# Kernel tuning notes

Measured on AMD Instinct MI355X. Metric: run time of the kernel, lower is better.

Reference implementation:

```python
import jax, jax.numpy as jnp
import numpy as np

B, S, D = 16, 512, 512
UPS = 3
THRESH = 1.0
SM1, NT1 = 1.0, 0.0
TAIL = 0.45
SM2, NT2 = 0.25, 0.01


def setup_inputs() -> dict:
    key = jax.random.key(0)
    ks = jax.random.split(key, 20)
    r = lambda k, sh, s: (jax.random.normal(k, sh, jnp.float32) * s)
    H4 = 4 * D
    return {
        "hidden": jax.random.normal(ks[0], (B, S, D), jnp.float32),
        "mask": jnp.ones((B, 1, S), jnp.float32),
        # Conv1d(D, D, 3): torch weight [out, in, k]
        "conv_w": r(ks[1], (D, D, 3), 0.03),
        "conv_b": jnp.zeros((D,), jnp.float32),
        # Linear(D, 1)
        "out_w": r(ks[2], (1, D), 0.05),
        "out_b": jnp.zeros((1,), jnp.float32),
        # ConvTranspose1d(D, D, 3, stride=3): torch weight [in, out, k]
        "up_w": r(ks[3], (D, D, 3), 0.03),
        "up_b": jnp.zeros((D,), jnp.float32),
        # BiLSTM(D -> D), torch gate order i,f,g,o
        "w_ih_f": r(ks[4], (H4, D), 0.03), "w_hh_f": r(ks[5], (H4, D), 0.03),
        "b_ih_f": jnp.zeros((H4,), jnp.float32), "b_hh_f": jnp.zeros((H4,), jnp.float32),
        "w_ih_b": r(ks[6], (H4, D), 0.03), "w_hh_b": r(ks[7], (H4, D), 0.03),
        "b_ih_b": jnp.zeros((H4,), jnp.float32), "b_hh_b": jnp.zeros((H4,), jnp.float32),
        # Linear(2D, 1)
        "out2_w": r(ks[8], (1, 2 * D), 0.05),
        "out2_b": jnp.zeros((1,), jnp.float32),
    }


def _lstm_dir(x, w_ih, w_hh, b_ih, b_hh, reverse):
    # x: [B, T, D] -> h: [B, T, H]
    Bx = x.shape[0]
    H = w_hh.shape[1]
    xg = jnp.einsum('btd,gd->btg', x, w_ih) + b_ih + b_hh  # [B,T,4H]
    xg = jnp.swapaxes(xg, 0, 1)  # [T,B,4H]

    def step(carry, g):
        h, c = carry
        g = g + h @ w_hh.T
        i, f, gg, o = jnp.split(g, 4, axis=-1)
        c = jax.nn.sigmoid(f) * c + jax.nn.sigmoid(i) * jnp.tanh(gg)
        h = jax.nn.sigmoid(o) * jnp.tanh(c)
        return (h, c), h

    init = (jnp.zeros((Bx, H), x.dtype), jnp.zeros((Bx, H), x.dtype))
    _, hs = jax.lax.scan(step, init, xg, reverse=reverse)
    return jnp.swapaxes(hs, 0, 1)


def _cif(h, alphas):
    # h: [B, T, D], alphas: [B, T] -> padded fired frames [B, T, D]
    Bz, Tz, Dz = h.shape

    def step(carry, inp):
        integrate, frame = carry
        alpha, h_t = inp
        dist = 1.0 - integrate
        integrate = integrate + alpha
        fire_val = integrate
        fire = integrate >= THRESH
        integrate = jnp.where(fire, integrate - 1.0, integrate)
        cur = jnp.where(fire, dist, alpha)
        frame_out = frame + cur[:, None] * h_t
        frame_next = jnp.where(fire[:, None], (alpha - cur)[:, None] * h_t, frame_out)
        return (integrate, frame_next), (fire_val, frame_out)

    init = (jnp.zeros((Bz,), h.dtype), jnp.zeros((Bz, Dz), h.dtype))
    xs = (jnp.swapaxes(alphas, 0, 1), jnp.swapaxes(h, 0, 1))
    _, (fires, frames) = jax.lax.scan(step, init, xs)
    fires = jnp.swapaxes(fires, 0, 1)    # [B,T]
    frames = jnp.swapaxes(frames, 0, 1)  # [B,T,D]
    # ragged gather of fired frames, packed to the front (vectorized)
    fire_mask = fires >= THRESH
    dest = jnp.where(fire_mask, jnp.cumsum(fire_mask.astype(jnp.int32), axis=1) - 1, Tz)
    embeds = jnp.zeros((Bz, Tz + 1, Dz), frames.dtype)
    embeds = embeds.at[jnp.arange(Bz)[:, None], dest].set(frames)
    return embeds[:, :Tz]  # drop dump slot


def _cif_wo_hidden(alphas):
    th = THRESH - 0.0001

    def step(integrate, alpha):
        integrate = integrate + alpha
        out = integrate
        integrate = jnp.where(integrate >= th, integrate - th, integrate)
        return integrate, out

    init = jnp.zeros((alphas.shape[0],), alphas.dtype)
    _, fires = jax.lax.scan(step, init, jnp.swapaxes(alphas, 0, 1))
    return jnp.swapaxes(fires, 0, 1)


def reference(hidden, mask, conv_w, conv_b, out_w, out_b, up_w, up_b,
              w_ih_f, w_hh_f, b_ih_f, b_hh_f, w_ih_b, w_hh_b, b_ih_b, b_hh_b,
              out2_w, out2_b):
    Bz, Sz, Dz = hidden.shape
    ctx = jnp.swapaxes(hidden, 1, 2)  # [B,D,S]
    # cif alphas branch: pad(1,1) + Conv1d(k=3) + relu
    q = jax.lax.conv_general_dilated(ctx, conv_w, (1,), [(1, 1)],
                                     dimension_numbers=('NCH', 'OIH', 'NCH'))
    q = jax.nn.relu(q + conv_b[None, :, None])
    out = jnp.swapaxes(q, 1, 2)  # [B,S,D]
    alphas = jax.nn.sigmoid(out @ out_w.T + out_b)        # [B,S,1]
    alphas = jax.nn.relu(alphas * SM1 - NT1)
    mk = jnp.swapaxes(mask, -1, -2)                        # [B,S,1]
    alphas = (alphas * mk)[..., 0]                         # [B,S]
    mk2 = mk[..., 0]                                       # [B,S]

    # tail_process_fn
    zeros_t = jnp.zeros((Bz, 1), alphas.dtype)
    ones_t = jnp.ones((Bz, 1), alphas.dtype)
    tail_mask = jnp.concatenate([ones_t, mk2], 1) - jnp.concatenate([mk2, zeros_t], 1)
    alphas = jnp.concatenate([alphas, zeros_t], 1) + tail_mask * TAIL  # [B,S+1]
    h = jnp.concatenate([hidden, jnp.zeros((Bz, 1, Dz), hidden.dtype)], 1)
    token_num = jnp.floor(jnp.sum(alphas, -1))

    acoustic_embeds = _cif(h, alphas)  # [B,S+1,D] (padded; original slices to max token_num)

    # get_timestamp: ConvTranspose1d stride==kernel==3 (non-overlapping)
    up = jnp.einsum('bit,iok->botk', ctx, up_w).reshape(Bz, Dz, Sz * UPS)
    up = up + up_b[None, :, None]
    xu = jnp.swapaxes(up, 1, 2)  # [B,3S,D]
    hf = _lstm_dir(xu, w_ih_f, w_hh_f, b_ih_f, b_hh_f, reverse=False)
    hb = _lstm_dir(xu, w_ih_b, w_hh_b, b_ih_b, b_hh_b, reverse=True)
    hcat = jnp.concatenate([hf, hb], -1)  # [B,3S,2D]
    us = jax.nn.sigmoid(hcat @ out2_w.T + out2_b)
    us = jax.nn.relu(us * SM2 - NT2)  # [B,3S,1]
    m_up = jnp.swapaxes(jnp.tile(mask, (1, UPS, 1)), -1, -2).reshape(Bz, -1)  # [B,3S]
    us_alphas = us[..., 0] * m_up
    us_alphas = us_alphas * (token_num / jnp.sum(us_alphas, -1))[:, None]
    us_peaks = _cif_wo_hidden(us_alphas)
    return acoustic_embeds, token_num, alphas, us_alphas, us_peaks
```

## Files before the change

kernel.cpp:

```cpp
#include <hip/hip_runtime.h>
#include <math.h>

constexpr int Bz = 16;
constexpr int Sz = 512;
constexpr int Dz = 512;
constexpr int T1 = Sz + 1;
constexpr int TU = Sz * 3;
constexpr float THRESHc = 1.0f;
constexpr float SM1c = 1.0f, NT1c = 0.0f;
constexpr float TAILc = 0.45f;
constexpr float SM2c = 0.25f, NT2c = 0.01f;

constexpr int GD = 16;

constexpr int EMB_OFF = 0;
constexpr int TOK_OFF = Bz * T1 * Dz;
constexpr int ALUT_OFF = TOK_OFF + Bz;
constexpr int USA_OFF = ALUT_OFF + Bz * T1;
constexpr int USP_OFF = USA_OFF + Bz * TU;

typedef short bf16x8 __attribute__((ext_vector_type(8)));
typedef float f32x4 __attribute__((ext_vector_type(4)));
typedef unsigned long long u64;

__device__ __forceinline__ float sigm(float x) { return 1.0f / (1.0f + expf(-x)); }
__device__ __forceinline__ float fsigm(float x) { return 1.0f / (1.0f + __expf(-x)); }
__device__ __forceinline__ float ftanh(float x) {
    float e = __expf(2.0f * x);
    return 1.0f - 2.0f / (e + 1.0f);
}
__device__ __forceinline__ unsigned short f2bf(float f) {
    unsigned u = __float_as_uint(f);
    return (unsigned short)((u + 0x7fffu + ((u >> 16) & 1u)) >> 16);
}

__global__ void k_transpose_convw(const float* __restrict__ cw, float* __restrict__ wt) {
    __shared__ float tile[64][65];
    int dt = blockIdx.x * 64, ct = blockIdx.y * 64;
    int tx = threadIdx.x & 63, ty = threadIdx.x >> 6;
    for (int r = ty; r < 64; r += 4)
        tile[r][tx] = cw[(dt + r) * 1536 + ct + tx];
    __syncthreads();
    for (int r = ty; r < 64; r += 4)
        wt[(ct + r) * 512 + dt + tx] = tile[tx][r];
}

__global__ void k_transpose_upw(const float* __restrict__ uw, float* __restrict__ upt) {
    __shared__ float tile[64][65];
    int it = blockIdx.x * 64, ct = blockIdx.y * 64;
    int tx = threadIdx.x & 63, ty = threadIdx.x >> 6;
    for (int r = ty; r < 64; r += 4)
        tile[r][tx] = uw[(it + r) * 1536 + ct + tx];
    __syncthreads();
    for (int r = ty; r < 64; r += 4) {
        int c = ct + r;
        int k = c % 3, o = c / 3;
        upt[(k * 512 + o) * 512 + it + tx] = tile[tx][r];
    }
}

__global__ void k_gconst(const float* __restrict__ wih_f, const float* __restrict__ bih_f,
                         const float* __restrict__ bhh_f, const float* __restrict__ wih_b,
                         const float* __restrict__ bih_b, const float* __restrict__ bhh_b,
                         const float* __restrict__ upb, float* __restrict__ gconst) {
    int g = blockIdx.x * 256 + threadIdx.x;
    int dir = g >> 11, gg = g & 2047;
    const float* wih = dir ? wih_b : wih_f;
    const float* bi = dir ? bih_b : bih_f;
    const float* bh = dir ? bhh_b : bhh_f;
    float s = bi[gg] + bh[gg];
    const float4* w4 = (const float4*)(wih + (size_t)gg * 512);
    const float4* u4 = (const float4*)upb;
    for (int o = 0; o < 128; ++o) {
        float4 w = w4[o], u = u4[o];
        s += w.x * u.x + w.y * u.y + w.z * u.z + w.w * u.w;
    }
    gconst[g] = s;
}

__global__ void k_M(const float* __restrict__ wih_f, const float* __restrict__ wih_b,
                    const float* __restrict__ upt, unsigned short* __restrict__ Mh) {
    __shared__ float As[32][68];
    __shared__ float Bs[32][68];
    int z = blockIdx.z;
    int dir = z / 3, k = z % 3;
    const float* A = dir ? wih_b : wih_f;
    const float* Bt = upt + (size_t)k * 262144;
    int g0 = blockIdx.y * 64, i0 = blockIdx.x * 64;
    int tid = threadIdx.x;
    int tx = tid & 15, ty = tid >> 4;
    float acc[4][4] = {};
    for (int k0 = 0; k0 < 512; k0 += 32) {
#pragma unroll
        for (int e = 0; e < 8; ++e) {
            int idx = e * 256 + tid;
            int ko = idx & 31, gl = idx >> 5;
            As[ko][gl] = A[(size_t)(g0 + gl) * 512 + k0 + ko];
        }
#pragma unroll
        for (int e = 0; e < 8; ++e) {
            int idx = e * 256 + tid;
            int il = idx & 63, ko = idx >> 6;
            Bs[ko][il] = Bt[(size_t)(k0 + ko) * 512 + i0 + il];
        }
        __syncthreads();
#pragma unroll
        for (int ko = 0; ko < 32; ++ko) {
            float4 a = *(const float4*)&As[ko][ty * 4];
            float4 b = *(const float4*)&Bs[ko][tx * 4];
            acc[0][0] += a.x * b.x; acc[0][1] += a.x * b.y; acc[0][2] += a.x * b.z; acc[0][3] += a.x * b.w;
            acc[1][0] += a.y * b.x; acc[1][1] += a.y * b.y; acc[1][2] += a.y * b.z; acc[1][3] += a.y * b.w;
            acc[2][0] += a.z * b.x; acc[2][1] += a.z * b.y; acc[2][2] += a.z * b.z; acc[2][3] += a.z * b.w;
            acc[3][0] += a.w * b.x; acc[3][1] += a.w * b.y; acc[3][2] += a.w * b.z; acc[3][3] += a.w * b.w;
        }
        __syncthreads();
    }
#pragma unroll
    for (int r = 0; r < 4; ++r) {
        ushort4 wh;
        wh.x = f2bf(acc[r][0]); wh.y = f2bf(acc[r][1]);
        wh.z = f2bf(acc[r][2]); wh.w = f2bf(acc[r][3]);
        *(ushort4*)&Mh[((size_t)(z * 2048 + g0 + ty * 4 + r)) * 512 + i0 + tx * 4] = wh;
    }
}

__global__ void k_Hbf(const float* __restrict__ hidden, unsigned short* __restrict__ Hs) {
    int i = blockIdx.x * 256 + threadIdx.x;
    float4 v = *(const float4*)&hidden[(size_t)i * 4];
    ushort4 h4;
    h4.x = f2bf(v.x); h4.y = f2bf(v.y); h4.z = f2bf(v.z); h4.w = f2bf(v.w);
    *(ushort4*)&Hs[(size_t)i * 4] = h4;
}

__global__ void k_conv_alpha(const float* __restrict__ hidden, const float* __restrict__ wt,
                             const float* __restrict__ cb, const float* __restrict__ ow,
                             const float* __restrict__ ob, const float* __restrict__ mask,
                             float* __restrict__ alph_s) {
    __shared__ float hs[18 * 512];
    __shared__ float red[16][257];
    int b = blockIdx.x, s0 = blockIdx.y * 16;
    int tid = threadIdx.x;
#pragma unroll
    for (int e = 0; e < 36; ++e) {
        int idx = e * 256 + tid;
        int r = idx >> 9, i = idx & 511;
        int s = s0 + r - 1;
        hs[idx] = (s >= 0 && s < Sz) ? hidden[((size_t)b * Sz + s) * Dz + i] : 0.f;
    }
    __syncthreads();
    float acc0[16] = {}, acc1[16] = {};
    int d0 = tid, d1 = tid + 256;
    for (int i = 0; i < 512; ++i) {
        float w00 = wt[(i * 3 + 0) * 512 + d0];
        float w01 = wt[(i * 3 + 1) * 512 + d0];
        float w02 = wt[(i * 3 + 2) * 512 + d0];
        float w10 = wt[(i * 3 + 0) * 512 + d1];
        float w11 = wt[(i * 3 + 1) * 512 + d1];
        float w12 = wt[(i * 3 + 2) * 512 + d1];
        float hv[18];
#pragma unroll
        for (int r = 0; r < 18; ++r) hv[r] = hs[r * 512 + i];
#pragma unroll
        for (int j = 0; j < 16; ++j) {
            acc0[j] += hv[j] * w00 + hv[j + 1] * w01 + hv[j + 2] * w02;
            acc1[j] += hv[j] * w10 + hv[j + 1] * w11 + hv[j + 2] * w12;
        }
    }
    float cb0 = cb[d0], cb1 = cb[d1], ow0 = ow[d0], ow1 = ow[d1];
#pragma unroll
    for (int j = 0; j < 16; ++j)
        red[j][tid] = fmaxf(acc0[j] + cb0, 0.f) * ow0 + fmaxf(acc1[j] + cb1, 0.f) * ow1;
    __syncthreads();
    for (int off = 128; off >= 1; off >>= 1) {
        if (tid < off) {
#pragma unroll
            for (int j = 0; j < 16; ++j) red[j][tid] += red[j][tid + off];
        }
        __syncthreads();
    }
    if (tid < 16) {
        float v = red[tid][0] + ob[0];
        float a = sigm(v);
        a = fmaxf(a * SM1c - NT1c, 0.f);
        a *= mask[b * Sz + s0 + tid];
        alph_s[b * Sz + s0 + tid] = a;
    }
}

__global__ void k_cif_scan(const float* __restrict__ alph_s, const float* __restrict__ mask,
                           float* __restrict__ out, float* __restrict__ sc_cur,
                           float* __restrict__ sc_res, int* __restrict__ sc_dst) {
    __shared__ float sa[16][T1];
    int tid = threadIdx.x;
    for (int idx = tid; idx < 16 * T1; idx += 256) {
        int b = idx / T1, t = idx % T1;
        float a = (t < Sz) ? alph_s[b * Sz + t] : 0.f;
        float mp = (t == 0) ? 1.f : mask[b * Sz + t - 1];
        float mc = (t < Sz) ? mask[b * Sz + t] : 0.f;
        sa[b][t] = a + (mp - mc) * TAILc;
    }
    __syncthreads();
    if (tid < 16) {
        int b = tid;
        float integ = 0.f, sum = 0.f;
        int nf = 0;
        for (int t = 0; t < T1; ++t) {
            float a = sa[b][t];
            out[ALUT_OFF + b * T1 + t] = a;
            sum += a;
            float dist = 1.f - integ;
            integ += a;
            bool fire = (integ >= THRESHc);
            float cur = fire ? dist : a;
            sc_cur[b * T1 + t] = cur;
            sc_res[b * T1 + t] = fire ? (a - cur) : 0.f;
            sc_dst[b * T1 + t] = fire ? (nf++) : -1;
            if (fire) integ -= 1.f;
        }
        out[TOK_OFF + b] = floorf(sum);
    }
}

__global__ void k_cif_frames(const float* __restrict__ hidden, const float* __restrict__ sc_cur,
                             const float* __restrict__ sc_res, const int* __restrict__ sc_dst,
                             float* __restrict__ out) {
    __shared__ float cu[T1], re[T1];
    __shared__ int dsx[T1];
    int b = blockIdx.x, d = blockIdx.y * 256 + threadIdx.x;
    for (int t = threadIdx.x; t < T1; t += 256) {
        cu[t] = sc_cur[b * T1 + t];
        re[t] = sc_res[b * T1 + t];
        dsx[t] = sc_dst[b * T1 + t];
    }
    __syncthreads();
    float frame = 0.f;
    for (int t = 0; t < T1; ++t) {
        float ht = (t < Sz) ? hidden[((size_t)b * Sz + t) * Dz + d] : 0.f;
        float f = frame + cu[t] * ht;
        int dst = dsx[t];
        if (dst >= 0) {
            out[EMB_OFF + ((size_t)b * T1 + dst) * Dz + d] = f;
            frame = re[t] * ht;
        } else {
            frame = f;
        }
    }
}

__global__ void __launch_bounds__(256, 1)
k_lstm(const unsigned short* __restrict__ Mh, const unsigned short* __restrict__ Hs,
       const float* __restrict__ whh_f, const float* __restrict__ whh_b,
       const float* __restrict__ gconst, const float* __restrict__ w2,
       unsigned short* hX, float* part, int* prog) {
    __shared__ unsigned short hbh[16 * 512];
    __shared__ float xch[3 * 256];

    const int wg = blockIdx.x;
    const int dir = wg >> 5, slice = wg & 31;
    const int d0 = slice * GD;
    const int tid = threadIdx.x;
    const int wv = tid >> 6;
    const int l = tid & 63;
    const int colb = l & 15;
    const int khi = l >> 4;
    const float* whh = dir ? whh_b : whh_f;

    bf16x8 whA[16];
    {
        const float* wr = whh + (size_t)(wv * 512 + d0 + colb) * 512 + khi * 8;
#pragma unroll
        for (int m = 0; m < 16; ++m) {
            float4 a = *(const float4*)(wr + m * 32);
            float4 b = *(const float4*)(wr + m * 32 + 4);
            union { unsigned short u[8]; bf16x8 v; } hh;
            hh.u[0] = f2bf(a.x); hh.u[1] = f2bf(a.y); hh.u[2] = f2bf(a.z); hh.u[3] = f2bf(a.w);
            hh.u[4] = f2bf(b.x); hh.u[5] = f2bf(b.y); hh.u[6] = f2bf(b.z); hh.u[7] = f2bf(b.w);
            whA[m] = hh.v;
        }
    }

    f32x4 bias;
    float w2v[4], cst[4] = {0.f, 0.f, 0.f, 0.f};
#pragma unroll
    for (int j = 0; j < 4; ++j) {
        bias[j] = gconst[dir * 2048 + wv * 512 + d0 + khi * 4 + j];
        w2v[j] = w2[dir * 512 + d0 + khi * 4 + j];
    }
    int* myprog = prog + (dir * 32 + slice) * 16;
    const int* pollp = prog + (dir * 32 + (l & 31)) * 16;

    auto idot = [&](int n) -> f32x4 {
        int t = dir ? (TU - 1 - n) : n;
        int s = t / 3, k = t - 3 * s;
        const unsigned short* ma = Mh + ((size_t)((dir * 3 + k) * 2048 + wv * 512 + d0 + colb)) * 512 + khi * 8;
        const unsigned short* xa = Hs + ((size_t)(colb * 512 + s)) * 512 + khi * 8;
        f32x4 a = bias;
#pragma unroll
        for (int m = 0; m < 16; ++m) {
            bf16x8 A = *(const bf16x8*)(ma + m * 32);
            bf16x8 B = *(const bf16x8*)(xa + m * 32);
            a = __builtin_amdgcn_mfma_f32_16x16x32_bf16(A, B, a, 0, 0, 0);
        }
        return a;
    };

    f32x4 accA = idot(0);

    for (int n = 0; n < TU; ++n) {
        int t = dir ? (TU - 1 - n) : n;
        if (n > 0) {
            {
                int it = 0;
                while (true) {
                    int v;
                    asm volatile("global_load_dword %0, %1, off sc0 sc1\n\ts_waitcnt vmcnt(0)"
                                 : "=v"(v) : "v"(pollp));
                    if (__ballot(v >= n) == ~0ull) break;
                    if (++it > (1 << 15)) break;
                    __builtin_amdgcn_s_sleep(1);
                }
            }
            int slot = (n - 1) & 1;
            const unsigned short* hb = hX + (size_t)((dir * 2 + slot) * 16) * 512;
            bf16x8 hg[4];
#pragma unroll
            for (int j = 0; j < 4; ++j)
                asm volatile("global_load_dwordx4 %0, %1, off sc0 sc1"
                             : "=v"(hg[j]) : "v"(hb + j * 2048 + tid * 8));
            asm volatile("s_waitcnt vmcnt(0)" ::: "memory");
            __builtin_amdgcn_sched_barrier(0);
#pragma unroll
            for (int j = 0; j < 4; ++j) {
                int row = j * 4 + wv;
                *(bf16x8*)&hbh[row * 512 + ((l ^ (row & 7)) * 8)] = hg[j];
            }
            __syncthreads();
#pragma unroll
            for (int m = 0; m < 16; ++m) {
                int G = m * 4 + khi;
                bf16x8 B = *(const bf16x8*)&hbh[colb * 512 + ((G ^ (colb & 7)) * 8)];
                accA = __builtin_amdgcn_mfma_f32_16x16x32_bf16(whA[m], B, accA, 0, 0, 0);
            }
        }
        if (wv != 0) {
#pragma unroll
            for (int j = 0; j < 4; ++j)
                xch[(wv - 1) * 256 + (khi * 4 + j) * 16 + colb] = accA[j];
        }
        __syncthreads();
        if (wv == 0) {
            unsigned short h4[4];
            float p = 0.f;
#pragma unroll
            for (int j = 0; j < 4; ++j) {
                int rr = khi * 4 + j;
                float gi = accA[j];
                float gf = xch[0 * 256 + rr * 16 + colb];
                float gg = xch[1 * 256 + rr * 16 + colb];
                float go = xch[2 * 256 + rr * 16 + colb];
                float c2 = fsigm(gf) * cst[j] + fsigm(gi) * ftanh(gg);
                cst[j] = c2;
                float h = fsigm(go) * ftanh(c2);
                h4[j] = f2bf(h);
                p += h * w2v[j];
            }
            u64 hq = (u64)h4[0] | ((u64)h4[1] << 16) | ((u64)h4[2] << 32) | ((u64)h4[3] << 48);
            size_t hoff = ((size_t)((dir * 2 + (n & 1)) * 16 + colb)) * 512 + d0 + khi * 4;
            asm volatile("global_store_dwordx2 %0, %1, off sc0 sc1"
                         :: "v"(hX + hoff), "v"(hq) : "memory");
            p += __shfl_xor(p, 16);
            p += __shfl_xor(p, 32);
            if (l < 16)
                part[((size_t)((dir * 32 + slice) * 16) + l) * TU + t] = p;
            asm volatile("s_waitcnt vmcnt(0)" ::: "memory");
            if (l == 0) {
                int nv = n + 1;
                asm volatile("global_store_dword %0, %1, off sc0 sc1"
                             :: "v"(myprog), "v"(nv) : "memory");
            }
        }
        accA = (n + 1 < TU) ? idot(n + 1) : bias;
    }
}

__global__ void k_us_reduce(const float* __restrict__ part, const float* __restrict__ ob2,
                            const float* __restrict__ mask, float* __restrict__ usA,
                            float* __restrict__ csum) {
    int b = blockIdx.x, ch = blockIdx.y;
    int t = ch * 256 + threadIdx.x;
    float s = 0.f;
#pragma unroll 8
    for (int p = 0; p < 64; ++p) s += part[((size_t)p * Bz + b) * TU + t];
    float u = sigm(s + ob2[0]);
    float ua = fmaxf(u * SM2c - NT2c, 0.f) * mask[b * Sz + t / 3];
    usA[b * TU + t] = ua;
    __shared__ float red[256];
    red[threadIdx.x] = ua;
    __syncthreads();
    for (int off = 128; off >= 1; off >>= 1) {
        if (threadIdx.x < off) red[threadIdx.x] += red[threadIdx.x + off];
        __syncthreads();
    }
    if (threadIdx.x == 0) csum[b * 6 + ch] = red[0];
}

__global__ void k_us_scan(const float* __restrict__ usA, const float* __restrict__ csum,
                          float* __restrict__ out) {
    __shared__ float ubuf[TU];
    int b = blockIdx.x;
    for (int t = threadIdx.x; t < TU; t += 64) ubuf[t] = usA[b * TU + t];
    __syncthreads();
    if (threadIdx.x == 0) {
        float tot = 0.f;
        for (int c = 0; c < 6; ++c) tot += csum[b * 6 + c];
        float scale = out[TOK_OFF + b] / tot;
        float integ = 0.f;
        const float th = THRESHc - 0.0001f;
        for (int t = 0; t < TU; ++t) {
            float ua = ubuf[t] * scale;
            out[USA_OFF + b * TU + t] = ua;
            integ += ua;
            out[USP_OFF + b * TU + t] = integ;
            if (integ >= th) integ -= th;
        }
    }
}

extern "C" void kernel_launch(void* const* d_in, const int* in_sizes, int n_in,
                              void* d_out, int out_size, void* d_ws, size_t ws_size,
                              hipStream_t stream) {
    const float* hidden = (const float*)d_in[0];
    const float* mask   = (const float*)d_in[1];
    const float* conv_w = (const float*)d_in[2];
    const float* conv_b = (const float*)d_in[3];
    const float* out_w  = (const float*)d_in[4];
    const float* out_b  = (const float*)d_in[5];
    const float* up_w   = (const float*)d_in[6];
    const float* up_b   = (const float*)d_in[7];
    const float* w_ih_f = (const float*)d_in[8];
    const float* w_hh_f = (const float*)d_in[9];
    const float* b_ih_f = (const float*)d_in[10];
    const float* b_hh_f = (const float*)d_in[11];
    const float* w_ih_b = (const float*)d_in[12];
    const float* w_hh_b = (const float*)d_in[13];
    const float* b_ih_b = (const float*)d_in[14];
    const float* b_hh_b = (const float*)d_in[15];
    const float* out2_w = (const float*)d_in[16];
    const float* out2_b = (const float*)d_in[17];
    float* out = (float*)d_out;
    float* ws = (float*)d_ws;

    float* wt     = ws + 0;
    float* upt    = ws + 786432;
    float* part   = ws + 1572864;
    float* gconst = ws + 3145728;
    float* alph_s = ws + 3149824;
    float* sc_cur = ws + 3158016;
    float* sc_res = ws + 3166224;
    int*   sc_dst = (int*)(ws + 3174432);
    unsigned short* hX = (unsigned short*)(ws + 3182640);
    float* usA    = ws + 3199024;
    float* csum   = ws + 3223600;
    int*   prog   = (int*)(ws + 3223696);
    unsigned short* Mh = (unsigned short*)(ws + 3224720);
    unsigned short* Hs = (unsigned short*)(ws + 6370448);

    hipMemsetAsync(out, 0, (size_t)Bz * T1 * Dz * sizeof(float), stream);
    hipMemsetAsync(prog, 0, 1024 * sizeof(int), stream);

    k_transpose_convw<<<dim3(8, 24), 256, 0, stream>>>(conv_w, wt);
    k_transpose_upw<<<dim3(8, 24), 256, 0, stream>>>(up_w, upt);
    k_gconst<<<16, 256, 0, stream>>>(w_ih_f, b_ih_f, b_hh_f, w_ih_b, b_ih_b, b_hh_b, up_b, gconst);
    k_M<<<dim3(8, 32, 6), 256, 0, stream>>>(w_ih_f, w_ih_b, upt, Mh);
    k_Hbf<<<4096, 256, 0, stream>>>(hidden, Hs);
    k_conv_alpha<<<dim3(16, 32), 256, 0, stream>>>(hidden, wt, conv_b, out_w, out_b, mask, alph_s);
    k_cif_scan<<<1, 256, 0, stream>>>(alph_s, mask, out, sc_cur, sc_res, sc_dst);
    k_cif_frames<<<dim3(16, 2), 256, 0, stream>>>(hidden, sc_cur, sc_res, sc_dst, out);

    {
        void* args[] = { (void*)&Mh, (void*)&Hs, (void*)&w_hh_f, (void*)&w_hh_b,
                         (void*)&gconst, (void*)&out2_w, (void*)&hX, (void*)&part,
                         (void*)&prog };
        hipLaunchCooperativeKernel(reinterpret_cast<void*>(&k_lstm), dim3(64), dim3(256),
                                   args, 0, stream);
    }

    k_us_reduce<<<dim3(16, 6), 256, 0, stream>>>(part, out2_b, mask, usA, csum);
    k_us_scan<<<16, 64, 0, stream>>>(usA, csum, out);
}
```

Before: 10.26 ms.

## Interleave both LSTM directions per workgroup and embed step tags in exchanged data

```diff
diff --git a/kernel.cpp b/kernel.cpp
--- a/kernel.cpp
+++ b/kernel.cpp
@@ -21,6 +21,7 @@
 
 typedef short bf16x8 __attribute__((ext_vector_type(8)));
 typedef float f32x4 __attribute__((ext_vector_type(4)));
+typedef unsigned u32x4 __attribute__((ext_vector_type(4)));
 typedef unsigned long long u64;
 
 __device__ __forceinline__ float sigm(float x) { return 1.0f / (1.0f + expf(-x)); }
@@ -251,50 +252,56 @@
 k_lstm(const unsigned short* __restrict__ Mh, const unsigned short* __restrict__ Hs,
        const float* __restrict__ whh_f, const float* __restrict__ whh_b,
        const float* __restrict__ gconst, const float* __restrict__ w2,
-       unsigned short* hX, float* part, int* prog) {
-    __shared__ unsigned short hbh[16 * 512];
+       u32x4* exch, float* part) {
+    __shared__ unsigned short hbuf[16 * 512];
     __shared__ float xch[3 * 256];
 
-    const int wg = blockIdx.x;
-    const int dir = wg >> 5, slice = wg & 31;
+    const int slice = blockIdx.x;
     const int d0 = slice * GD;
     const int tid = threadIdx.x;
     const int wv = tid >> 6;
     const int l = tid & 63;
     const int colb = l & 15;
     const int khi = l >> 4;
-    const float* whh = dir ? whh_b : whh_f;
-
-    bf16x8 whA[16];
+
+    bf16x8 whF[16], whB[16];
     {
-        const float* wr = whh + (size_t)(wv * 512 + d0 + colb) * 512 + khi * 8;
+        const float* wrF = whh_f + (size_t)(wv * 512 + d0 + colb) * 512 + khi * 8;
+        const float* wrB = whh_b + (size_t)(wv * 512 + d0 + colb) * 512 + khi * 8;
 #pragma unroll
         for (int m = 0; m < 16; ++m) {
-            float4 a = *(const float4*)(wr + m * 32);
-            float4 b = *(const float4*)(wr + m * 32 + 4);
-            union { unsigned short u[8]; bf16x8 v; } hh;
-            hh.u[0] = f2bf(a.x); hh.u[1] = f2bf(a.y); hh.u[2] = f2bf(a.z); hh.u[3] = f2bf(a.w);
-            hh.u[4] = f2bf(b.x); hh.u[5] = f2bf(b.y); hh.u[6] = f2bf(b.z); hh.u[7] = f2bf(b.w);
-            whA[m] = hh.v;
-        }
-    }
-
-    f32x4 bias;
-    float w2v[4], cst[4] = {0.f, 0.f, 0.f, 0.f};
+            float4 a = *(const float4*)(wrF + m * 32);
+            float4 b = *(const float4*)(wrF + m * 32 + 4);
+            union { unsigned short u[8]; bf16x8 v; } t1;
+            t1.u[0] = f2bf(a.x); t1.u[1] = f2bf(a.y); t1.u[2] = f2bf(a.z); t1.u[3] = f2bf(a.w);
+            t1.u[4] = f2bf(b.x); t1.u[5] = f2bf(b.y); t1.u[6] = f2bf(b.z); t1.u[7] = f2bf(b.w);
+            whF[m] = t1.v;
+            a = *(const float4*)(wrB + m * 32);
+            b = *(const float4*)(wrB + m * 32 + 4);
+            union { unsigned short u[8]; bf16x8 v; } t2;
+            t2.u[0] = f2bf(a.x); t2.u[1] = f2bf(a.y); t2.u[2] = f2bf(a.z); t2.u[3] = f2bf(a.w);
+            t2.u[4] = f2bf(b.x); t2.u[5] = f2bf(b.y); t2.u[6] = f2bf(b.z); t2.u[7] = f2bf(b.w);
+            whB[m] = t2.v;
+        }
+    }
+
+    f32x4 biasF, biasB;
+    float w2F[4], w2B[4];
+    f32x4 cstF = {0.f, 0.f, 0.f, 0.f}, cstB = {0.f, 0.f, 0.f, 0.f};
 #pragma unroll
     for (int j = 0; j < 4; ++j) {
-        bias[j] = gconst[dir * 2048 + wv * 512 + d0 + khi * 4 + j];
-        w2v[j] = w2[dir * 512 + d0 + khi * 4 + j];
-    }
-    int* myprog = prog + (dir * 32 + slice) * 16;
-    const int* pollp = prog + (dir * 32 + (l & 31)) * 16;
-
-    auto idot = [&](int n) -> f32x4 {
+        biasF[j] = gconst[0 * 2048 + wv * 512 + d0 + khi * 4 + j];
+        biasB[j] = gconst[1 * 2048 + wv * 512 + d0 + khi * 4 + j];
+        w2F[j] = w2[0 * 512 + d0 + khi * 4 + j];
+        w2B[j] = w2[1 * 512 + d0 + khi * 4 + j];
+    }
+
+    auto idot = [&](int dir, int n) -> f32x4 {
         int t = dir ? (TU - 1 - n) : n;
         int s = t / 3, k = t - 3 * s;
         const unsigned short* ma = Mh + ((size_t)((dir * 3 + k) * 2048 + wv * 512 + d0 + colb)) * 512 + khi * 8;
         const unsigned short* xa = Hs + ((size_t)(colb * 512 + s)) * 512 + khi * 8;
-        f32x4 a = bias;
+        f32x4 a = dir ? biasB : biasF;
 #pragma unroll
         for (int m = 0; m < 16; ++m) {
             bf16x8 A = *(const bf16x8*)(ma + m * 32);
@@ -304,48 +311,57 @@
         return a;
     };
 
-    f32x4 accA = idot(0);
-
-    for (int n = 0; n < TU; ++n) {
-        int t = dir ? (TU - 1 - n) : n;
-        if (n > 0) {
-            {
-                int it = 0;
-                while (true) {
-                    int v;
-                    asm volatile("global_load_dword %0, %1, off sc0 sc1\n\ts_waitcnt vmcnt(0)"
-                                 : "=v"(v) : "v"(pollp));
-                    if (__ballot(v >= n) == ~0ull) break;
-                    if (++it > (1 << 15)) break;
-                    __builtin_amdgcn_s_sleep(1);
-                }
-            }
-            int slot = (n - 1) & 1;
-            const unsigned short* hb = hX + (size_t)((dir * 2 + slot) * 16) * 512;
-            bf16x8 hg[4];
+    u32x4 gS[8];
+
+    auto issue8 = [&](int d, int n) {
+        const u32x4* base = exch + (size_t)((d * 2 + ((n - 1) & 1)) * 2048) + tid * 8;
+#pragma unroll
+        for (int j = 0; j < 8; ++j)
+            asm volatile("global_load_dwordx4 %0, %1, off sc0 sc1"
+                         : "=v"(gS[j]) : "v"(base + j));
+    };
+    auto waitok = [&](int d, int n) {
+        const u32x4* base = exch + (size_t)((d * 2 + ((n - 1) & 1)) * 2048) + tid * 8;
+        unsigned tag = (unsigned)n;
+        int it = 0;
+        while (true) {
+            asm volatile("s_waitcnt vmcnt(0)" ::: "memory");
+            bool ok = true;
+#pragma unroll
+            for (int j = 0; j < 8; ++j) ok = ok && (gS[j][2] == tag);
+            if (__ballot(!ok) == 0ull) break;
+            if (++it > (1 << 13)) break;
+            __builtin_amdgcn_s_sleep(1);
+#pragma unroll
+            for (int j = 0; j < 8; ++j)
+                asm volatile("global_load_dwordx4 %0, %1, off sc0 sc1"
+                             : "=v"(gS[j]) : "v"(base + j));
+        }
+    };
+    auto unpack = [&]() {
+#pragma unroll
+        for (int j = 0; j < 8; ++j) {
+            int u = tid * 8 + j;
+            int batch = u & 15;
+            int gq = u >> 4;
+            int sw = (((gq >> 1) ^ (batch & 7)) << 3) + ((gq & 1) << 2);
+            u64 q = (u64)gS[j][0] | ((u64)gS[j][1] << 32);
+            *(u64*)&hbuf[batch * 512 + sw] = q;
+        }
+    };
+    auto hhdot = [&](const bf16x8* wh, f32x4 acc) -> f32x4 {
+#pragma unroll
+        for (int m = 0; m < 16; ++m) {
+            bf16x8 B = *(const bf16x8*)&hbuf[colb * 512 + (((m * 4 + khi) ^ (colb & 7)) << 3)];
+            acc = __builtin_amdgcn_mfma_f32_16x16x32_bf16(wh[m], B, acc, 0, 0, 0);
+        }
+        return acc;
+    };
+    auto cellphase = [&](f32x4 acc, f32x4& cst, const float* w2v, int d, int n, int t) {
+        if (wv != 0) {
 #pragma unroll
             for (int j = 0; j < 4; ++j)
-                asm volatile("global_load_dwordx4 %0, %1, off sc0 sc1"
-                             : "=v"(hg[j]) : "v"(hb + j * 2048 + tid * 8));
-            asm volatile("s_waitcnt vmcnt(0)" ::: "memory");
-            __builtin_amdgcn_sched_barrier(0);
-#pragma unroll
-            for (int j = 0; j < 4; ++j) {
-                int row = j * 4 + wv;
-                *(bf16x8*)&hbh[row * 512 + ((l ^ (row & 7)) * 8)] = hg[j];
-            }
-            __syncthreads();
-#pragma unroll
-            for (int m = 0; m < 16; ++m) {
-                int G = m * 4 + khi;
-                bf16x8 B = *(const bf16x8*)&hbh[colb * 512 + ((G ^ (colb & 7)) * 8)];
-                accA = __builtin_amdgcn_mfma_f32_16x16x32_bf16(whA[m], B, accA, 0, 0, 0);
-            }
-        }
-        if (wv != 0) {
-#pragma unroll
-            for (int j = 0; j < 4; ++j)
-                xch[(wv - 1) * 256 + (khi * 4 + j) * 16 + colb] = accA[j];
+                xch[(wv - 1) * 256 + (khi * 4 + j) * 16 + colb] = acc[j];
         }
         __syncthreads();
         if (wv == 0) {
@@ -354,7 +370,7 @@
 #pragma unroll
             for (int j = 0; j < 4; ++j) {
                 int rr = khi * 4 + j;
-                float gi = accA[j];
+                float gi = acc[j];
                 float gf = xch[0 * 256 + rr * 16 + colb];
                 float gg = xch[1 * 256 + rr * 16 + colb];
                 float go = xch[2 * 256 + rr * 16 + colb];
@@ -364,22 +380,43 @@
                 h4[j] = f2bf(h);
                 p += h * w2v[j];
             }
-            u64 hq = (u64)h4[0] | ((u64)h4[1] << 16) | ((u64)h4[2] << 32) | ((u64)h4[3] << 48);
-            size_t hoff = ((size_t)((dir * 2 + (n & 1)) * 16 + colb)) * 512 + d0 + khi * 4;
-            asm volatile("global_store_dwordx2 %0, %1, off sc0 sc1"
-                         :: "v"(hX + hoff), "v"(hq) : "memory");
+            unsigned lo = (unsigned)h4[0] | ((unsigned)h4[1] << 16);
+            unsigned hi = (unsigned)h4[2] | ((unsigned)h4[3] << 16);
+            u32x4 outv = { lo, hi, (unsigned)(n + 1), (unsigned)(n + 1) };
+            u32x4* dst = exch + (size_t)((d * 2 + (n & 1)) * 2048 + slice * 64 + l);
+            asm volatile("global_store_dwordx4 %0, %1, off sc0 sc1"
+                         :: "v"(dst), "v"(outv) : "memory");
             p += __shfl_xor(p, 16);
             p += __shfl_xor(p, 32);
             if (l < 16)
-                part[((size_t)((dir * 32 + slice) * 16) + l) * TU + t] = p;
-            asm volatile("s_waitcnt vmcnt(0)" ::: "memory");
-            if (l == 0) {
-                int nv = n + 1;
-                asm volatile("global_store_dword %0, %1, off sc0 sc1"
-                             :: "v"(myprog), "v"(nv) : "memory");
-            }
-        }
-        accA = (n + 1 < TU) ? idot(n + 1) : bias;
+                part[((size_t)((d * 32 + slice) * 16) + l) * TU + t] = p;
+        }
+    };
+
+    f32x4 accF = idot(0, 0);
+    f32x4 accB = idot(1, 0);
+
+    for (int n = 0; n < TU; ++n) {
+        if (n > 0) {
+            waitok(0, n);
+            unpack();
+            __syncthreads();
+            accF = hhdot(whF, accF);
+        }
+        cellphase(accF, cstF, w2F, 0, n, n);
+        if (n > 0) issue8(1, n);
+        if (n + 1 < TU) accF = idot(0, n + 1);
+        if (n > 0) {
+            waitok(1, n);
+            unpack();
+            __syncthreads();
+            accB = hhdot(whB, accB);
+        }
+        cellphase(accB, cstB, w2B, 1, n, TU - 1 - n);
+        if (n + 1 < TU) {
+            issue8(0, n + 1);
+            accB = idot(1, n + 1);
+        }
     }
 }
 
@@ -458,15 +495,14 @@
     float* sc_cur = ws + 3158016;
     float* sc_res = ws + 3166224;
     int*   sc_dst = (int*)(ws + 3174432);
-    unsigned short* hX = (unsigned short*)(ws + 3182640);
-    float* usA    = ws + 3199024;
-    float* csum   = ws + 3223600;
-    int*   prog   = (int*)(ws + 3223696);
-    unsigned short* Mh = (unsigned short*)(ws + 3224720);
-    unsigned short* Hs = (unsigned short*)(ws + 6370448);
+    float* usA    = ws + 3182640;
+    float* csum   = ws + 3207216;
+    unsigned short* Mh = (unsigned short*)(ws + 3207312);
+    unsigned short* Hs = (unsigned short*)(ws + 6353040);
+    u32x4* exch   = (u32x4*)(ws + 8450192);
 
     hipMemsetAsync(out, 0, (size_t)Bz * T1 * Dz * sizeof(float), stream);
-    hipMemsetAsync(prog, 0, 1024 * sizeof(int), stream);
+    hipMemsetAsync(exch, 0, 8192 * 16, stream);
 
     k_transpose_convw<<<dim3(8, 24), 256, 0, stream>>>(conv_w, wt);
     k_transpose_upw<<<dim3(8, 24), 256, 0, stream>>>(up_w, upt);
@@ -479,9 +515,8 @@
 
     {
         void* args[] = { (void*)&Mh, (void*)&Hs, (void*)&w_hh_f, (void*)&w_hh_b,
-                         (void*)&gconst, (void*)&out2_w, (void*)&hX, (void*)&part,
-                         (void*)&prog };
-        hipLaunchCooperativeKernel(reinterpret_cast<void*>(&k_lstm), dim3(64), dim3(256),
+                         (void*)&gconst, (void*)&out2_w, (void*)&exch, (void*)&part };
+        hipLaunchCooperativeKernel(reinterpret_cast<void*>(&k_lstm), dim3(32), dim3(256),
                                    args, 0, stream);
     }
 
```

New measurement: 18.51 ms. +80.3%, slower.

## Halve LSTM workgroups with 32 hidden units each and spread gate math across waves

Applied to the files above, without the earlier changes.

```diff
diff --git a/kernel.cpp b/kernel.cpp
--- a/kernel.cpp
+++ b/kernel.cpp
@@ -11,7 +11,8 @@
 constexpr float TAILc = 0.45f;
 constexpr float SM2c = 0.25f, NT2c = 0.01f;
 
-constexpr int GD = 16;
+constexpr int SLD = 16;
+constexpr int GD = 32;
 
 constexpr int EMB_OFF = 0;
 constexpr int TOK_OFF = Bz * T1 * Dz;
@@ -252,11 +253,13 @@
        const float* __restrict__ whh_f, const float* __restrict__ whh_b,
        const float* __restrict__ gconst, const float* __restrict__ w2,
        unsigned short* hX, float* part, int* prog) {
-    __shared__ unsigned short hbh[16 * 512];
-    __shared__ float xch[3 * 256];
+    __shared__ unsigned short hbuf[16 * 512];
+    __shared__ float xch[4 * 32 * 17];
+    __shared__ float pbuf[32 * 17];
+    __shared__ unsigned short hout[16 * 32];
 
     const int wg = blockIdx.x;
-    const int dir = wg >> 5, slice = wg & 31;
+    const int dir = wg >> 4, slice = wg & 15;
     const int d0 = slice * GD;
     const int tid = threadIdx.x;
     const int wv = tid >> 6;
@@ -265,9 +268,10 @@
     const int khi = l >> 4;
     const float* whh = dir ? whh_b : whh_f;
 
-    bf16x8 whA[16];
-    {
-        const float* wr = whh + (size_t)(wv * 512 + d0 + colb) * 512 + khi * 8;
+    bf16x8 whA0[16], whA1[16];
+#pragma unroll
+    for (int rt = 0; rt < 2; ++rt) {
+        const float* wr = whh + (size_t)(wv * 512 + d0 + rt * 16 + colb) * 512 + khi * 8;
 #pragma unroll
         for (int m = 0; m < 16; ++m) {
             float4 a = *(const float4*)(wr + m * 32);
@@ -275,36 +279,44 @@
             union { unsigned short u[8]; bf16x8 v; } hh;
             hh.u[0] = f2bf(a.x); hh.u[1] = f2bf(a.y); hh.u[2] = f2bf(a.z); hh.u[3] = f2bf(a.w);
             hh.u[4] = f2bf(b.x); hh.u[5] = f2bf(b.y); hh.u[6] = f2bf(b.z); hh.u[7] = f2bf(b.w);
-            whA[m] = hh.v;
-        }
-    }
-
-    f32x4 bias;
-    float w2v[4], cst[4] = {0.f, 0.f, 0.f, 0.f};
+            if (rt == 0) whA0[m] = hh.v; else whA1[m] = hh.v;
+        }
+    }
+
+    f32x4 bias0, bias1;
 #pragma unroll
     for (int j = 0; j < 4; ++j) {
-        bias[j] = gconst[dir * 2048 + wv * 512 + d0 + khi * 4 + j];
-        w2v[j] = w2[dir * 512 + d0 + khi * 4 + j];
-    }
-    int* myprog = prog + (dir * 32 + slice) * 16;
-    const int* pollp = prog + (dir * 32 + (l & 31)) * 16;
-
-    auto idot = [&](int n) -> f32x4 {
+        bias0[j] = gconst[dir * 2048 + wv * 512 + d0 + khi * 4 + j];
+        bias1[j] = gconst[dir * 2048 + wv * 512 + d0 + 16 + khi * 4 + j];
+    }
+    const int cb = tid >> 4;
+    const int cd0 = (tid & 15) * 2;
+    const float w20 = w2[dir * 512 + d0 + cd0];
+    const float w21 = w2[dir * 512 + d0 + cd0 + 1];
+    float cs0 = 0.f, cs1 = 0.f;
+
+    int* myprog = prog + (dir * SLD + slice) * 16;
+    const int* pollp = prog + (dir * SLD + (l & 15)) * 16;
+
+    auto idot = [&](int n, f32x4& a0, f32x4& a1) {
         int t = dir ? (TU - 1 - n) : n;
         int s = t / 3, k = t - 3 * s;
-        const unsigned short* ma = Mh + ((size_t)((dir * 3 + k) * 2048 + wv * 512 + d0 + colb)) * 512 + khi * 8;
+        const unsigned short* ma0 = Mh + ((size_t)((dir * 3 + k) * 2048 + wv * 512 + d0 + colb)) * 512 + khi * 8;
+        const unsigned short* ma1 = ma0 + (size_t)16 * 512;
         const unsigned short* xa = Hs + ((size_t)(colb * 512 + s)) * 512 + khi * 8;
-        f32x4 a = bias;
+        a0 = bias0; a1 = bias1;
 #pragma unroll
         for (int m = 0; m < 16; ++m) {
-            bf16x8 A = *(const bf16x8*)(ma + m * 32);
             bf16x8 B = *(const bf16x8*)(xa + m * 32);
-            a = __builtin_amdgcn_mfma_f32_16x16x32_bf16(A, B, a, 0, 0, 0);
-        }
-        return a;
+            bf16x8 A0 = *(const bf16x8*)(ma0 + m * 32);
+            bf16x8 A1 = *(const bf16x8*)(ma1 + m * 32);
+            a0 = __builtin_amdgcn_mfma_f32_16x16x32_bf16(A0, B, a0, 0, 0, 0);
+            a1 = __builtin_amdgcn_mfma_f32_16x16x32_bf16(A1, B, a1, 0, 0, 0);
+        }
     };
 
-    f32x4 accA = idot(0);
+    f32x4 acc0, acc1;
+    idot(0, acc0, acc1);
 
     for (int n = 0; n < TU; ++n) {
         int t = dir ? (TU - 1 - n) : n;
@@ -317,61 +329,64 @@
                                  : "=v"(v) : "v"(pollp));
                     if (__ballot(v >= n) == ~0ull) break;
                     if (++it > (1 << 15)) break;
-                    __builtin_amdgcn_s_sleep(1);
                 }
             }
-            int slot = (n - 1) & 1;
-            const unsigned short* hb = hX + (size_t)((dir * 2 + slot) * 16) * 512;
-            bf16x8 hg[4];
-#pragma unroll
-            for (int j = 0; j < 4; ++j)
-                asm volatile("global_load_dwordx4 %0, %1, off sc0 sc1"
-                             : "=v"(hg[j]) : "v"(hb + j * 2048 + tid * 8));
+            const unsigned short* hb = hX + (size_t)((dir * 2 + ((n - 1) & 1)) * 16 + (tid >> 4)) * 512 + (tid & 15) * 32;
+            bf16x8 g0, g1, g2, g3;
+            asm volatile("global_load_dwordx4 %0, %1, off sc0 sc1" : "=v"(g0) : "v"(hb));
+            asm volatile("global_load_dwordx4 %0, %1, off sc0 sc1" : "=v"(g1) : "v"(hb + 8));
+            asm volatile("global_load_dwordx4 %0, %1, off sc0 sc1" : "=v"(g2) : "v"(hb + 16));
+            asm volatile("global_load_dwordx4 %0, %1, off sc0 sc1" : "=v"(g3) : "v"(hb + 24));
             asm volatile("s_waitcnt vmcnt(0)" ::: "memory");
             __builtin_amdgcn_sched_barrier(0);
-#pragma unroll
-            for (int j = 0; j < 4; ++j) {
-                int row = j * 4 + wv;
-                *(bf16x8*)&hbh[row * 512 + ((l ^ (row & 7)) * 8)] = hg[j];
+            {
+                int batch = tid >> 4, ch = tid & 15;
+                int gq = ch * 4;
+                *(bf16x8*)&hbuf[batch * 512 + (((gq + 0) ^ (batch & 7)) << 3)] = g0;
+                *(bf16x8*)&hbuf[batch * 512 + (((gq + 1) ^ (batch & 7)) << 3)] = g1;
+                *(bf16x8*)&hbuf[batch * 512 + (((gq + 2) ^ (batch & 7)) << 3)] = g2;
+                *(bf16x8*)&hbuf[batch * 512 + (((gq + 3) ^ (batch & 7)) << 3)] = g3;
             }
             __syncthreads();
 #pragma unroll
             for (int m = 0; m < 16; ++m) {
-                int G = m * 4 + khi;
-                bf16x8 B = *(const bf16x8*)&hbh[colb * 512 + ((G ^ (colb & 7)) * 8)];
-                accA = __builtin_amdgcn_mfma_f32_16x16x32_bf16(whA[m], B, accA, 0, 0, 0);
+                bf16x8 B = *(const bf16x8*)&hbuf[colb * 512 + (((m * 4 + khi) ^ (colb & 7)) << 3)];
+                acc0 = __builtin_amdgcn_mfma_f32_16x16x32_bf16(whA0[m], B, acc0, 0, 0, 0);
+                acc1 = __builtin_amdgcn_mfma_f32_16x16x32_bf16(whA1[m], B, acc1, 0, 0, 0);
             }
         }
-        if (wv != 0) {
-#pragma unroll
-            for (int j = 0; j < 4; ++j)
-                xch[(wv - 1) * 256 + (khi * 4 + j) * 16 + colb] = accA[j];
+#pragma unroll
+        for (int j = 0; j < 4; ++j) {
+            xch[wv * 544 + (khi * 4 + j) * 17 + colb] = acc0[j];
+            xch[wv * 544 + (16 + khi * 4 + j) * 17 + colb] = acc1[j];
+        }
+        __syncthreads();
+        {
+            float gi0 = xch[0 * 544 + cd0 * 17 + cb];
+            float gf0 = xch[1 * 544 + cd0 * 17 + cb];
+            float gg0 = xch[2 * 544 + cd0 * 17 + cb];
+            float go0 = xch[3 * 544 + cd0 * 17 + cb];
+            float gi1 = xch[0 * 544 + (cd0 + 1) * 17 + cb];
+            float gf1 = xch[1 * 544 + (cd0 + 1) * 17 + cb];
+            float gg1 = xch[2 * 544 + (cd0 + 1) * 17 + cb];
+            float go1 = xch[3 * 544 + (cd0 + 1) * 17 + cb];
+            float c0 = fsigm(gf0) * cs0 + fsigm(gi0) * ftanh(gg0);
+            float c1 = fsigm(gf1) * cs1 + fsigm(gi1) * ftanh(gg1);
+            cs0 = c0; cs1 = c1;
+            float h0 = fsigm(go0) * ftanh(c0);
+            float h1 = fsigm(go1) * ftanh(c1);
+            unsigned hw = (unsigned)f2bf(h0) | ((unsigned)f2bf(h1) << 16);
+            *(unsigned*)&hout[cb * 32 + cd0] = hw;
+            pbuf[cd0 * 17 + cb] = h0 * w20;
+            pbuf[(cd0 + 1) * 17 + cb] = h1 * w21;
         }
         __syncthreads();
         if (wv == 0) {
-            unsigned short h4[4];
-            float p = 0.f;
-#pragma unroll
-            for (int j = 0; j < 4; ++j) {
-                int rr = khi * 4 + j;
-                float gi = accA[j];
-                float gf = xch[0 * 256 + rr * 16 + colb];
-                float gg = xch[1 * 256 + rr * 16 + colb];
-                float go = xch[2 * 256 + rr * 16 + colb];
-                float c2 = fsigm(gf) * cst[j] + fsigm(gi) * ftanh(gg);
-                cst[j] = c2;
-                float h = fsigm(go) * ftanh(c2);
-                h4[j] = f2bf(h);
-                p += h * w2v[j];
-            }
-            u64 hq = (u64)h4[0] | ((u64)h4[1] << 16) | ((u64)h4[2] << 32) | ((u64)h4[3] << 48);
-            size_t hoff = ((size_t)((dir * 2 + (n & 1)) * 16 + colb)) * 512 + d0 + khi * 4;
-            asm volatile("global_store_dwordx2 %0, %1, off sc0 sc1"
-                         :: "v"(hX + hoff), "v"(hq) : "memory");
-            p += __shfl_xor(p, 16);
-            p += __shfl_xor(p, 32);
-            if (l < 16)
-                part[((size_t)((dir * 32 + slice) * 16) + l) * TU + t] = p;
+            int b = l >> 2, g4 = l & 3;
+            bf16x8 hv = *(const bf16x8*)&hout[b * 32 + g4 * 8];
+            unsigned short* dst = hX + (size_t)((dir * 2 + (n & 1)) * 16 + b) * 512 + d0 + g4 * 8;
+            asm volatile("global_store_dwordx4 %0, %1, off sc0 sc1"
+                         :: "v"(dst), "v"(hv) : "memory");
             asm volatile("s_waitcnt vmcnt(0)" ::: "memory");
             if (l == 0) {
                 int nv = n + 1;
@@ -379,7 +394,13 @@
                              :: "v"(myprog), "v"(nv) : "memory");
             }
         }
-        accA = (n + 1 < TU) ? idot(n + 1) : bias;
+        if (wv == 1 && l < 16) {
+            float s = 0.f;
+#pragma unroll
+            for (int d = 0; d < 32; ++d) s += pbuf[d * 17 + l];
+            part[((size_t)((dir * SLD + slice) * 16) + l) * TU + t] = s;
+        }
+        if (n + 1 < TU) idot(n + 1, acc0, acc1);
     }
 }
 
@@ -390,7 +411,7 @@
     int t = ch * 256 + threadIdx.x;
     float s = 0.f;
 #pragma unroll 8
-    for (int p = 0; p < 64; ++p) s += part[((size_t)p * Bz + b) * TU + t];
+    for (int p = 0; p < 32; ++p) s += part[((size_t)p * Bz + b) * TU + t];
     float u = sigm(s + ob2[0]);
     float ua = fmaxf(u * SM2c - NT2c, 0.f) * mask[b * Sz + t / 3];
     usA[b * TU + t] = ua;
@@ -458,12 +479,12 @@
     float* sc_cur = ws + 3158016;
     float* sc_res = ws + 3166224;
     int*   sc_dst = (int*)(ws + 3174432);
-    unsigned short* hX = (unsigned short*)(ws + 3182640);
-    float* usA    = ws + 3199024;
-    float* csum   = ws + 3223600;
-    int*   prog   = (int*)(ws + 3223696);
-    unsigned short* Mh = (unsigned short*)(ws + 3224720);
-    unsigned short* Hs = (unsigned short*)(ws + 6370448);
+    float* usA    = ws + 3182640;
+    float* csum   = ws + 3207216;
+    unsigned short* Mh = (unsigned short*)(ws + 3207312);
+    unsigned short* Hs = (unsigned short*)(ws + 6353040);
+    unsigned short* hX = (unsigned short*)(ws + 8450192);
+    int*   prog   = (int*)(ws + 8482960);
 
     hipMemsetAsync(out, 0, (size_t)Bz * T1 * Dz * sizeof(float), stream);
     hipMemsetAsync(prog, 0, 1024 * sizeof(int), stream);
@@ -481,7 +502,7 @@
         void* args[] = { (void*)&Mh, (void*)&Hs, (void*)&w_hh_f, (void*)&w_hh_b,
                          (void*)&gconst, (void*)&out2_w, (void*)&hX, (void*)&part,
                          (void*)&prog };
-        hipLaunchCooperativeKernel(reinterpret_cast<void*>(&k_lstm), dim3(64), dim3(256),
+        hipLaunchCooperativeKernel(reinterpret_cast<void*>(&k_lstm), dim3(32), dim3(256),
                                    args, 0, stream);
     }
 
```

Result: slower. 12.67 ms (+23.4%).
